# Kernel optimization log

Measured on AMD Instinct MI355X. Metric: run time of the kernel, lower is better.

Reference implementation:

```python
import jax, jax.numpy as jnp
import numpy as np

N, E, H, HEADS, NC, BLK = 100000, 1600000, 128, 4, 8192, 128

def _layernorm(x, g, b, eps=1e-5):
    m = jnp.mean(x, axis=-1, keepdims=True)
    v = jnp.var(x, axis=-1, keepdims=True)
    return (x - m) * jax.lax.rsqrt(v + eps) * g + b

def setup_inputs() -> dict:
    key = jax.random.key(0)
    ks = jax.random.split(key, 24)
    s = 0.05
    p = lambda k, shp: jax.random.normal(k, shp, jnp.float32) * s
    return {
        'x': jax.random.normal(ks[0], (N, H), jnp.float32),
        'ea': jax.random.normal(ks[1], (E, H), jnp.float32),
        # GINEConv edge linear (edge_dim -> hidden)
        'We': p(ks[2], (H, H)), 'be_': p(ks[3], (H,)),
        # GINEConv mlp: Linear(H,H) -> ReLU -> Linear(H,H)
        'W1': p(ks[4], (H, H)), 'b1': p(ks[5], (H,)),
        'W2': p(ks[6], (H, H)), 'b2': p(ks[7], (H,)),
        'ln1_g': jnp.ones((H,), jnp.float32), 'ln1_b': jnp.zeros((H,), jnp.float32),
        # MultiheadAttention packed qkv + out proj
        'in_w': p(ks[8], (3 * H, H)), 'in_b': p(ks[9], (3 * H,)),
        'out_w': p(ks[10], (H, H)), 'out_b': p(ks[11], (H,)),
        'ln2_g': jnp.ones((H,), jnp.float32), 'ln2_b': jnp.zeros((H,), jnp.float32),
        # FFN: Linear(H,2H) -> ReLU -> Linear(2H,H)
        'f1_w': p(ks[12], (2 * H, H)), 'f1_b': p(ks[13], (2 * H,)),
        'f2_w': p(ks[14], (H, 2 * H)), 'f2_b': p(ks[15], (H,)),
        'ei': jax.random.randint(ks[16], (2, E), 0, N, jnp.int64),
        'chem_idx': jnp.arange(NC, dtype=jnp.int64),
        'B': BLK,
    }

def reference(x, ea, We, be_, W1, b1, W2, b2, ln1_g, ln1_b, in_w, in_b,
              out_w, out_b, ln2_g, ln2_b, f1_w, f1_b, f2_w, f2_b,
              ei, chem_idx, B):
    n = x.shape[0]
    # ---- GINEConv: out_i = mlp((1+eps)*x_i + sum_j relu(x_j + lin(e_ji))), eps=0 ----
    src, dst = ei[0], ei[1]
    msg = jax.nn.relu(x[src] + ea @ We.T + be_)          # [E, H]
    agg = jax.ops.segment_sum(msg, dst, num_segments=n)  # [N, H]
    h = agg + x
    h = jax.nn.relu(h @ W1.T + b1) @ W2.T + b2
    x = _layernorm(x + h, ln1_g, ln1_b)
    # ---- chunked self-attention over chem nodes (chunks of size B) ----
    xc = x[chem_idx].reshape(-1, B, x.shape[-1])         # [nc, B, H]
    nc, _, hid = xc.shape
    dh = hid // HEADS
    qkv = xc @ in_w.T + in_b                             # [nc, B, 3H]
    q, k, v = jnp.split(qkv, 3, axis=-1)
    sp = lambda t: t.reshape(nc, B, HEADS, dh)
    att = jax.nn.softmax(jnp.einsum('bqhd,bkhd->bhqk', sp(q), sp(k)) * (1.0 / np.sqrt(dh)).astype(np.float32), axis=-1)
    o = jnp.einsum('bhqk,bkhd->bqhd', att, sp(v)).reshape(nc, B, hid)
    xc = xc + (o @ out_w.T + out_b)                      # residual inside BlockMHA
    xc = xc.reshape(-1, hid)
    # ---- FFN on chem subset ----
    h2 = _layernorm(xc, ln2_g, ln2_b)
    xc = xc + (jax.nn.relu(h2 @ f1_w.T + f1_b) @ f2_w.T + f2_b)
    return x.at[chem_idx].set(xc)
```

## Files before the change

### kernel.cpp

```cpp
#include <hip/hip_runtime.h>
#include <hip/hip_bf16.h>
#include <math.h>

typedef __attribute__((ext_vector_type(8))) __bf16 bf16x8;
typedef __attribute__((ext_vector_type(4))) float f32x4;
typedef __attribute__((ext_vector_type(4))) unsigned short u16x4;

#define HD  128
#define LDP 136

__device__ __forceinline__ unsigned short f2bf(float f) {
  __bf16 h = (__bf16)f;
  union { __bf16 h; unsigned short u; } v; v.h = h; return v.u;
}
__device__ __forceinline__ float bf2f(unsigned short h) {
  union { unsigned u; float f; } v; v.u = ((unsigned)h) << 16; return v.f;
}

__device__ __forceinline__ int idx_at(const void* p, long long i, int is64) {
  if (is64) return (int)((const long long*)p)[i];
  return ((const int*)p)[i];
}

__device__ __forceinline__ void mfma_tile_128(const unsigned short* a_s,
                                              const unsigned short* w_s,
                                              int w, int l15, int lg,
                                              f32x4 acc[2][8]) {
#pragma unroll
  for (int kk = 0; kk < 4; ++kk) {
    bf16x8 a[2], b[8];
#pragma unroll
    for (int mt = 0; mt < 2; ++mt)
      a[mt] = *(const bf16x8*)&a_s[(w * 32 + mt * 16 + l15) * LDP + kk * 32 + lg * 8];
#pragma unroll
    for (int nt = 0; nt < 8; ++nt)
      b[nt] = *(const bf16x8*)&w_s[(nt * 16 + l15) * LDP + kk * 32 + lg * 8];
#pragma unroll
    for (int mt = 0; mt < 2; ++mt)
#pragma unroll
      for (int nt = 0; nt < 8; ++nt)
        acc[mt][nt] = __builtin_amdgcn_mfma_f32_16x16x32_bf16(a[mt], b[nt], acc[mt][nt], 0, 0, 0);
  }
}

__device__ __forceinline__ void mfma_tile_gb(const unsigned short* a_s,
                                             const unsigned short* Wb,
                                             int w, int l15, int lg,
                                             f32x4 acc[2][8]) {
#pragma unroll
  for (int kk = 0; kk < 4; ++kk) {
    bf16x8 a[2], b[8];
#pragma unroll
    for (int mt = 0; mt < 2; ++mt)
      a[mt] = *(const bf16x8*)&a_s[(w * 32 + mt * 16 + l15) * LDP + kk * 32 + lg * 8];
#pragma unroll
    for (int nt = 0; nt < 8; ++nt)
      b[nt] = *(const bf16x8*)&Wb[(nt * 16 + l15) * 128 + kk * 32 + lg * 8];
#pragma unroll
    for (int mt = 0; mt < 2; ++mt)
#pragma unroll
      for (int nt = 0; nt < 8; ++nt)
        acc[mt][nt] = __builtin_amdgcn_mfma_f32_16x16x32_bf16(a[mt], b[nt], acc[mt][nt], 0, 0, 0);
  }
}

__device__ __forceinline__ void stage_f32s(unsigned short* dst, const float* src,
                                           long long src_ld, int tid, int T) {
  for (int i = tid; i < 128 * 32; i += T) {
    int r = i >> 5, c = (i & 31) << 2;
    float4 f = *(const float4*)&src[(long long)r * src_ld + c];
    u16x4 h = { f2bf(f.x), f2bf(f.y), f2bf(f.z), f2bf(f.w) };
    *(u16x4*)&dst[r * LDP + c] = h;
  }
}

__global__ void detect_idx_kernel(const void* __restrict__ ei, int E, int N,
                                  int* __restrict__ flag) {
  if (threadIdx.x == 0 && blockIdx.x == 0) {
    const long long* p = (const long long*)ei;
    int is64 = 1;
    long long step = E / 64; if (step < 1) step = 1;
    for (int i = 0; i < 64; ++i) {
      long long v = p[i * step];
      if (v < 0 || v >= N) { is64 = 0; break; }
    }
    *flag = is64;
  }
}

__global__ __launch_bounds__(256) void conv_we_kernel(const float* __restrict__ We,
                                                      unsigned short* __restrict__ we_bf) {
  int i = blockIdx.x * 256 + threadIdx.x;
  if (i < 128 * 128) {
    int r = i >> 7, c = i & 127;
    we_bf[r * 136 + c] = f2bf(We[i]);
  }
}
__global__ __launch_bounds__(256) void conv_w_kernel(const float* __restrict__ W,
                                                     unsigned short* __restrict__ out,
                                                     int n) {
  int i = blockIdx.x * 256 + threadIdx.x;
  if (i < n) out[i] = f2bf(W[i]);
}
__global__ __launch_bounds__(256) void conv_x_kernel(const float* __restrict__ x,
                                                     unsigned short* __restrict__ xb,
                                                     long long n8) {
  long long i = blockIdx.x * 256LL + threadIdx.x;
  if (i < n8) {
    float4 f0 = *(const float4*)&x[i * 8];
    float4 f1 = *(const float4*)&x[i * 8 + 4];
    u16x4 h0 = { f2bf(f0.x), f2bf(f0.y), f2bf(f0.z), f2bf(f0.w) };
    u16x4 h1 = { f2bf(f1.x), f2bf(f1.y), f2bf(f1.z), f2bf(f1.w) };
    *(u16x4*)&xb[i * 8] = h0;
    *(u16x4*)&xb[i * 8 + 4] = h1;
  }
}

__global__ __launch_bounds__(256) void hist_kernel(const void* __restrict__ ei,
                                                   const int* __restrict__ flag,
                                                   int* __restrict__ deg, int E) {
  const int is64 = *flag;
  for (long long e = blockIdx.x * 256LL + threadIdx.x; e < E;
       e += (long long)gridDim.x * 256)
    atomicAdd(&deg[idx_at(ei, (long long)E + e, is64)], 1);
}

#define SCH 1024
__global__ __launch_bounds__(256) void scan_a(const int* __restrict__ deg,
                                              int* __restrict__ bsum, int N) {
  const int b = blockIdx.x, t = threadIdx.x;
  int p = 0;
#pragma unroll
  for (int k = 0; k < 4; ++k) {
    int idx = b * SCH + t * 4 + k;
    if (idx < N) p += deg[idx];
  }
  __shared__ int warr[4];
  for (int o = 32; o > 0; o >>= 1) p += __shfl_xor(p, o);
  if ((t & 63) == 0) warr[t >> 6] = p;
  __syncthreads();
  if (t == 0) bsum[b] = warr[0] + warr[1] + warr[2] + warr[3];
}
__global__ void scan_b(int* __restrict__ bsum, int* __restrict__ off, int NB, int N) {
  if (threadIdx.x == 0 && blockIdx.x == 0) {
    int run = 0;
    for (int b = 0; b < NB; ++b) { int t = bsum[b]; bsum[b] = run; run += t; }
    off[N] = run;
  }
}
__global__ __launch_bounds__(128) void scan_b2(int* __restrict__ bsum,
                                               int* __restrict__ off, int NB, int N) {
  __shared__ int arr[128];
  const int t = threadIdx.x;
  int v = (t < NB) ? bsum[t] : 0;
  arr[t] = v;
  __syncthreads();
  for (int s = 1; s < 128; s <<= 1) {
    int u = (t >= s) ? arr[t - s] : 0;
    __syncthreads();
    arr[t] += u;
    __syncthreads();
  }
  if (t < NB) bsum[t] = arr[t] - v;
  if (t == 0) off[N] = arr[127];
}
__global__ __launch_bounds__(256) void scan_c(const int* __restrict__ deg,
                                              const int* __restrict__ bsum,
                                              int* __restrict__ off,
                                              int* __restrict__ cursor, int N) {
  const int b = blockIdx.x, t = threadIdx.x;
  int d[4], s = 0;
#pragma unroll
  for (int k = 0; k < 4; ++k) {
    int idx = b * SCH + t * 4 + k;
    d[k] = (idx < N) ? deg[idx] : 0;
    s += d[k];
  }
  __shared__ int arr[256];
  arr[t] = s;
  __syncthreads();
  for (int stp = 1; stp < 256; stp <<= 1) {
    int v = (t >= stp) ? arr[t - stp] : 0;
    __syncthreads();
    arr[t] += v;
    __syncthreads();
// ... 106 lines not shown
    bf16x8 g = *(const bf16x8*)&we_s[r * LDP + sg * 8];
    u16x4 h0, h1;
#pragma unroll
    for (int k = 0; k < 4; ++k) {
      float v = (float)g[k] + (float)xv[k];
      h0[k] = f2bf(v > 0.f ? v : 0.f);
    }
#pragma unroll
    for (int k = 0; k < 4; ++k) {
      float v = (float)g[4 + k] + (float)xv[4 + k];
      h1[k] = f2bf(v > 0.f ? v : 0.f);
    }
    unsigned short* mp = &msg[(size_t)s_pos[r] * 128 + sg * 8];
    *(u16x4*)&mp[0] = h0;
    *(u16x4*)&mp[4] = h1;
  }
}

__global__ __launch_bounds__(256) void gather_kernel(
    const unsigned short* __restrict__ x_bf, const int* __restrict__ off,
    const unsigned short* __restrict__ msg, unsigned short* __restrict__ h_bf,
    int N) {
  const int tid = threadIdx.x;
  const int grp = tid >> 4, li = tid & 15;
  const long long row = (long long)blockIdx.x * 16 + grp;
  if (row >= N) return;
  const int co = li * 8;
  float a8[8];
  bf16x8 xv = *(const bf16x8*)&x_bf[row * HD + co];
#pragma unroll
  for (int k = 0; k < 8; ++k) a8[k] = (float)xv[k];
  const int j0 = off[row], j1 = off[row + 1];
  int j = j0;
  for (; j + 3 < j1; j += 4) {
    bf16x8 v0 = *(const bf16x8*)&msg[(size_t)j * 128 + co];
    bf16x8 v1 = *(const bf16x8*)&msg[(size_t)(j + 1) * 128 + co];
    bf16x8 v2 = *(const bf16x8*)&msg[(size_t)(j + 2) * 128 + co];
    bf16x8 v3 = *(const bf16x8*)&msg[(size_t)(j + 3) * 128 + co];
#pragma unroll
    for (int k = 0; k < 8; ++k)
      a8[k] += ((float)v0[k] + (float)v1[k]) + ((float)v2[k] + (float)v3[k]);
  }
  for (; j < j1; ++j) {
    bf16x8 v0 = *(const bf16x8*)&msg[(size_t)j * 128 + co];
#pragma unroll
    for (int k = 0; k < 8; ++k) a8[k] += (float)v0[k];
  }
  bf16x8 hv;
#pragma unroll
  for (int k = 0; k < 8; ++k) hv[k] = (__bf16)a8[k];
  *(bf16x8*)&h_bf[row * HD + co] = hv;
}

__global__ __launch_bounds__(256, 4) void mlp_kernel(
    const float* __restrict__ x, float* __restrict__ xo,
    const unsigned short* __restrict__ h_bf,
    const unsigned short* __restrict__ W1b, const float* __restrict__ b1,
    const unsigned short* __restrict__ W2b, const float* __restrict__ b2,
    const float* __restrict__ g1, const float* __restrict__ bt1, int N) {
  __shared__ unsigned short a_s[128 * LDP];
  const int tid = threadIdx.x;
  const long long r0 = (long long)blockIdx.x * 128;

  for (int i = tid; i < 2048; i += 256) {
    int r = i >> 4, c = (i & 15) << 3;
    long long gr = r0 + r;
    bf16x8 v;
    if (gr < N) v = *(const bf16x8*)&h_bf[gr * HD + c];
    else {
#pragma unroll
      for (int k = 0; k < 8; ++k) v[k] = (__bf16)0.f;
    }
    *(bf16x8*)&a_s[r * LDP + c] = v;
  }
  __syncthreads();

  const int lane = tid & 63, w = tid >> 6;
  const int l15 = lane & 15, lg = lane >> 4;
  f32x4 acc[2][8];
#pragma unroll
  for (int mt = 0; mt < 2; ++mt)
#pragma unroll
    for (int nt = 0; nt < 8; ++nt) acc[mt][nt] = (f32x4){0.f, 0.f, 0.f, 0.f};
  mfma_tile_gb(a_s, W1b, w, l15, lg, acc);
  __syncthreads();

#pragma unroll
  for (int mt = 0; mt < 2; ++mt)
#pragma unroll
    for (int r = 0; r < 4; ++r) {
      int m = w * 32 + mt * 16 + lg * 4 + r;
#pragma unroll
      for (int nt = 0; nt < 8; ++nt) {
        int n = nt * 16 + l15;
        float t = acc[mt][nt][r] + b1[n];
        a_s[m * LDP + n] = f2bf(t > 0.f ? t : 0.f);
      }
    }
  __syncthreads();

  f32x4 acc2[2][8];
#pragma unroll
  for (int mt = 0; mt < 2; ++mt)
#pragma unroll
    for (int nt = 0; nt < 8; ++nt) acc2[mt][nt] = (f32x4){0.f, 0.f, 0.f, 0.f};
  mfma_tile_gb(a_s, W2b, w, l15, lg, acc2);
  __syncthreads();

#pragma unroll
  for (int mt = 0; mt < 2; ++mt)
#pragma unroll
    for (int r = 0; r < 4; ++r) {
      int m = w * 32 + mt * 16 + lg * 4 + r;
      if (r0 + m < N) {
#pragma unroll
        for (int nt = 0; nt < 8; ++nt) {
          int n = nt * 16 + l15;
          a_s[m * LDP + n] = f2bf(x[(r0 + m) * HD + n] + acc2[mt][nt][r] + b2[n]);
        }
      }
    }
  __syncthreads();

  for (int row = w; row < 128; row += 4) {
    if (r0 + row >= N) continue;
    float v1 = bf2f(a_s[row * LDP + lane]), v2 = bf2f(a_s[row * LDP + 64 + lane]);
    float s = v1 + v2, sq = v1 * v1 + v2 * v2;
    for (int o = 32; o > 0; o >>= 1) { s += __shfl_xor(s, o); sq += __shfl_xor(sq, o); }
    float mean = s * (1.f / 128.f);
    float var = sq * (1.f / 128.f) - mean * mean;
    float rs = rsqrtf(var + 1e-5f);
    xo[(r0 + row) * HD + lane]      = (v1 - mean) * rs * g1[lane] + bt1[lane];
    xo[(r0 + row) * HD + 64 + lane] = (v2 - mean) * rs * g1[lane + 64] + bt1[lane + 64];
  }
}

__global__ __launch_bounds__(256) void edge_kernel(
    const float* __restrict__ x, const float* __restrict__ ea,
    const float* __restrict__ We, const float* __restrict__ be,
    const void* __restrict__ ei, const int* __restrict__ flag,
    float* __restrict__ agg, int E, int N) {
  __shared__ unsigned short ea_s[128 * LDP];
  __shared__ unsigned short we_s[128 * LDP];
  __shared__ int s_src[128];
  __shared__ int s_dst[128];
  const int tid = threadIdx.x;
  const long long e0 = (long long)blockIdx.x * 128;
  const int is64 = *flag;
  if (tid < 128) {
    long long e = e0 + tid;
    int s = 0, d = 0;
    if (e < E) { s = idx_at(ei, e, is64); d = idx_at(ei, (long long)E + e, is64); }
    s_src[tid] = s; s_dst[tid] = d;
  }
  for (int i = tid; i < 128 * 32; i += 256) {
    int r = i >> 5, c = (i & 31) << 2;
    float4 f = {0.f, 0.f, 0.f, 0.f};
    if (e0 + r < E) f = *(const float4*)&ea[(e0 + r) * HD + c];
    u16x4 h = { f2bf(f.x), f2bf(f.y), f2bf(f.z), f2bf(f.w) };
    *(u16x4*)&ea_s[r * LDP + c] = h;
    float4 g = *(const float4*)&We[r * HD + c];
    u16x4 hw = { f2bf(g.x), f2bf(g.y), f2bf(g.z), f2bf(g.w) };
    *(u16x4*)&we_s[r * LDP + c] = hw;
  }
  __syncthreads();
  const int lane = tid & 63, w = tid >> 6;
  const int l15 = lane & 15, lg = lane >> 4;
  f32x4 acc[2][8];
#pragma unroll
  for (int mt = 0; mt < 2; ++mt)
#pragma unroll
    for (int nt = 0; nt < 8; ++nt) acc[mt][nt] = (f32x4){0.f, 0.f, 0.f, 0.f};
  mfma_tile_128(ea_s, we_s, w, l15, lg, acc);
  float bev[8];
#pragma unroll
  for (int nt = 0; nt < 8; ++nt) bev[nt] = be[nt * 16 + l15];
#pragma unroll
  for (int mt = 0; mt < 2; ++mt) {
#pragma unroll
    for (int r = 0; r < 4; ++r) {
      int m = w * 32 + mt * 16 + lg * 4 + r;
      if (e0 + m >= E) continue;
      const float* xrow = x + (size_t)s_src[m] * HD;
      float* arow = agg + (size_t)s_dst[m] * HD;
#pragma unroll
      for (int nt = 0; nt < 8; ++nt) {
        int n = nt * 16 + l15;
        float val = acc[mt][nt][r] + bev[nt] + xrow[n];
        if (val > 0.f) unsafeAtomicAdd(&arow[n], val);
      }
    }
  }
}

__global__ __launch_bounds__(256) void node_kernel(
    const float* __restrict__ x, float* xo,
    const float* __restrict__ W1, const float* __restrict__ b1,
    const float* __restrict__ W2, const float* __restrict__ b2,
    const float* __restrict__ g1, const float* __restrict__ bt1, int N) {
  __shared__ char smem[2 * 128 * LDP * 2];
  unsigned short* a_s = (unsigned short*)smem;
  unsigned short* w_s = (unsigned short*)smem + 128 * LDP;
  float* y_s = (float*)smem;
  const int tid = threadIdx.x;
  const long long r0 = (long long)blockIdx.x * 128;
  for (int i = tid; i < 128 * 32; i += 256) {
    int r = i >> 5, c = (i & 31) << 2;
    float4 f = {0.f, 0.f, 0.f, 0.f};
    if (r0 + r < N) {
      float4 xa = *(const float4*)&x[(r0 + r) * HD + c];
      float4 ag = *(const float4*)&xo[(r0 + r) * HD + c];
      f.x = xa.x + ag.x; f.y = xa.y + ag.y; f.z = xa.z + ag.z; f.w = xa.w + ag.w;
    }
    u16x4 h = { f2bf(f.x), f2bf(f.y), f2bf(f.z), f2bf(f.w) };
    *(u16x4*)&a_s[r * LDP + c] = h;
    float4 g = *(const float4*)&W1[r * HD + c];
    u16x4 hw = { f2bf(g.x), f2bf(g.y), f2bf(g.z), f2bf(g.w) };
    *(u16x4*)&w_s[r * LDP + c] = hw;
  }
  __syncthreads();
  const int lane = tid & 63, w = tid >> 6;
  const int l15 = lane & 15, lg = lane >> 4;
  f32x4 acc[2][8];
#pragma unroll
  for (int mt = 0; mt < 2; ++mt)
#pragma unroll
    for (int nt = 0; nt < 8; ++nt) acc[mt][nt] = (f32x4){0.f, 0.f, 0.f, 0.f};
  mfma_tile_128(a_s, w_s, w, l15, lg, acc);
  __syncthreads();
#pragma unroll
  for (int mt = 0; mt < 2; ++mt)
#pragma unroll
    for (int r = 0; r < 4; ++r) {
      int m = w * 32 + mt * 16 + lg * 4 + r;
#pragma unroll
      for (int nt = 0; nt < 8; ++nt) {
        int n = nt * 16 + l15;
        float t = acc[mt][nt][r] + b1[n];
        a_s[m * LDP + n] = f2bf(t > 0.f ? t : 0.f);
      }
    }
  stage_f32s(w_s, W2, HD, tid, 256);
  __syncthreads();
  f32x4 acc2[2][8];
#pragma unroll
  for (int mt = 0; mt < 2; ++mt)
#pragma unroll
    for (int nt = 0; nt < 8; ++nt) acc2[mt][nt] = (f32x4){0.f, 0.f, 0.f, 0.f};
  mfma_tile_128(a_s, w_s, w, l15, lg, acc2);
  __syncthreads();
#pragma unroll
  for (int mt = 0; mt < 2; ++mt)
#pragma unroll
    for (int r = 0; r < 4; ++r) {
      int m = w * 32 + mt * 16 + lg * 4 + r;
      if (r0 + m < N) {
#pragma unroll
        for (int nt = 0; nt < 8; ++nt) {
          int n = nt * 16 + l15;
          y_s[m * 132 + n] = x[(r0 + m) * HD + n] + acc2[mt][nt][r] + b2[n];
        }
      }
    }
  __syncthreads();
  for (int row = w; row < 128; row += 4) {
    if (r0 + row >= N) continue;
    float v1 = y_s[row * 132 + lane], v2 = y_s[row * 132 + 64 + lane];
    float s = v1 + v2, sq = v1 * v1 + v2 * v2;
    for (int o = 32; o > 0; o >>= 1) { s += __shfl_xor(s, o); sq += __shfl_xor(sq, o); }
    float mean = s * (1.f / 128.f);
    float var = sq * (1.f / 128.f) - mean * mean;
    float rs = rsqrtf(var + 1e-5f);
    xo[(r0 + row) * HD + lane]      = (v1 - mean) * rs * g1[lane] + bt1[lane];
    xo[(r0 + row) * HD + 64 + lane] = (v2 - mean) * rs * g1[lane + 64] + bt1[lane + 64];
  }
}

__global__ __launch_bounds__(256) void qkv_kernel(
    const float* __restrict__ xo, const float* __restrict__ in_w,
    const float* __restrict__ in_b, const void* __restrict__ chem,
    const int* __restrict__ flag, float* __restrict__ qkv) {
  __shared__ unsigned short a_s[128 * LDP];
  __shared__ unsigned short w_s[128 * LDP];
  __shared__ int s_row[128];
  const int tid = threadIdx.x;
  const int chunk = blockIdx.x, sec = blockIdx.y;
  const int is64 = *flag;
  if (tid < 128) s_row[tid] = idx_at(chem, (long long)chunk * 128 + tid, is64);
  __syncthreads();
  for (int i = tid; i < 128 * 32; i += 256) {
    int r = i >> 5, c = (i & 31) << 2;
    float4 f = *(const float4*)&xo[(size_t)s_row[r] * HD + c];
    u16x4 h = { f2bf(f.x), f2bf(f.y), f2bf(f.z), f2bf(f.w) };
    *(u16x4*)&a_s[r * LDP + c] = h;
    float4 g = *(const float4*)&in_w[(size_t)(sec * 128 + r) * HD + c];
    u16x4 hw = { f2bf(g.x), f2bf(g.y), f2bf(g.z), f2bf(g.w) };
    *(u16x4*)&w_s[r * LDP + c] = hw;
  }
  __syncthreads();
  const int lane = tid & 63, w = tid >> 6;
  const int l15 = lane & 15, lg = lane >> 4;
  f32x4 acc[2][8];
#pragma unroll
  for (int mt = 0; mt < 2; ++mt)
#pragma unroll
    for (int nt = 0; nt < 8; ++nt) acc[mt][nt] = (f32x4){0.f, 0.f, 0.f, 0.f};
  mfma_tile_128(a_s, w_s, w, l15, lg, acc);
#pragma unroll
  for (int mt = 0; mt < 2; ++mt)
#pragma unroll
    for (int r = 0; r < 4; ++r) {
      int m = w * 32 + mt * 16 + lg * 4 + r;
#pragma unroll
      for (int nt = 0; nt < 8; ++nt) {
        int n = nt * 16 + l15;
        qkv[(size_t)(chunk * 128 + m) * 384 + sec * 128 + n] = acc[mt][nt][r] + in_b[sec * 128 + n];
      }
    }
}

__global__ __launch_bounds__(128) void attn_kernel(const float* __restrict__ qkv,
                                                   float* __restrict__ o) {
  __shared__ float k_s[128 * 32];
  __shared__ float v_s[128 * 32];
  const int tid = threadIdx.x;
  const int chunk = blockIdx.x, h = blockIdx.y;
  const float scale = 0.1767766952966369f;
  for (int i = tid; i < 128 * 32; i += 128) {
    int r = i >> 5, d = i & 31;
    k_s[i] = qkv[(size_t)(chunk * 128 + r) * 384 + 128 + h * 32 + d];
    v_s[i] = qkv[(size_t)(chunk * 128 + r) * 384 + 256 + h * 32 + d];
  }
  float qr[32];
  const int m = tid;
#pragma unroll
  for (int d = 0; d < 32; ++d)
    qr[d] = qkv[(size_t)(chunk * 128 + m) * 384 + h * 32 + d] * scale;
  __syncthreads();
  float mx = -1e30f, sm = 0.f;
  for (int j = 0; j < 128; ++j) {
    float s = 0.f;
#pragma unroll
    for (int d = 0; d < 32; ++d) s += qr[d] * k_s[j * 32 + d];
    if (s > mx) { sm = sm * __expf(mx - s); mx = s; }
    sm += __expf(s - mx);
  }
  const float inv = 1.f / sm;
  float ov[32];
#pragma unroll
  for (int d = 0; d < 32; ++d) ov[d] = 0.f;
  for (int j = 0; j < 128; ++j) {
    float s = 0.f;
#pragma unroll
    for (int d = 0; d < 32; ++d) s += qr[d] * k_s[j * 32 + d];
    float p = __expf(s - mx) * inv;
#pragma unroll
    for (int d = 0; d < 32; ++d) ov[d] += p * v_s[j * 32 + d];
  }
#pragma unroll
  for (int d = 0; d < 32; ++d)
    o[(size_t)(chunk * 128 + m) * HD + h * 32 + d] = ov[d];
}

__global__ __launch_bounds__(256) void oproj_kernel(
    const float* __restrict__ xo, const float* __restrict__ o,
    const float* __restrict__ Wo, const float* __restrict__ bo,
    const float* __restrict__ g2, const float* __restrict__ bt2,
    const void* __restrict__ chem, const int* __restrict__ flag,
    float* __restrict__ xc2, unsigned short* __restrict__ h2b) {
  __shared__ char smem[2 * 128 * LDP * 2];
  unsigned short* a_s = (unsigned short*)smem;
  unsigned short* w_s = (unsigned short*)smem + 128 * LDP;
  float* y_s = (float*)smem;
  __shared__ int s_row[128];
  const int tid = threadIdx.x;
  const int chunk = blockIdx.x;
  const int is64 = *flag;
  if (tid < 128) s_row[tid] = idx_at(chem, (long long)chunk * 128 + tid, is64);
  stage_f32s(a_s, o + (size_t)chunk * 128 * HD, HD, tid, 256);
  stage_f32s(w_s, Wo, HD, tid, 256);
  __syncthreads();
  const int lane = tid & 63, w = tid >> 6;
  const int l15 = lane & 15, lg = lane >> 4;
  f32x4 acc[2][8];
#pragma unroll
  for (int mt = 0; mt < 2; ++mt)
#pragma unroll
    for (int nt = 0; nt < 8; ++nt) acc[mt][nt] = (f32x4){0.f, 0.f, 0.f, 0.f};
  mfma_tile_128(a_s, w_s, w, l15, lg, acc);
  __syncthreads();
#pragma unroll
  for (int mt = 0; mt < 2; ++mt)
#pragma unroll
    for (int r = 0; r < 4; ++r) {
      int m = w * 32 + mt * 16 + lg * 4 + r;
#pragma unroll
      for (int nt = 0; nt < 8; ++nt) {
        int n = nt * 16 + l15;
        y_s[m * 132 + n] = xo[(size_t)s_row[m] * HD + n] + acc[mt][nt][r] + bo[n];
      }
    }
  __syncthreads();
  for (int row = w; row < 128; row += 4) {
    float v1 = y_s[row * 132 + lane], v2 = y_s[row * 132 + 64 + lane];
    float s = v1 + v2, sq = v1 * v1 + v2 * v2;
    for (int o2 = 32; o2 > 0; o2 >>= 1) { s += __shfl_xor(s, o2); sq += __shfl_xor(sq, o2); }
    float mean = s * (1.f / 128.f);
    float var = sq * (1.f / 128.f) - mean * mean;
    float rs = rsqrtf(var + 1e-5f);
    size_t gi = (size_t)(chunk * 128 + row) * HD;
    xc2[gi + lane] = v1; xc2[gi + 64 + lane] = v2;
    h2b[gi + lane]      = f2bf((v1 - mean) * rs * g2[lane] + bt2[lane]);
    h2b[gi + 64 + lane] = f2bf((v2 - mean) * rs * g2[lane + 64] + bt2[lane + 64]);
  }
}

__global__ __launch_bounds__(256) void ffn1_kernel(
    const unsigned short* __restrict__ h2b, const float* __restrict__ f1w,
    const float* __restrict__ f1b, unsigned short* __restrict__ u) {
  __shared__ unsigned short a_s[128 * LDP];
  __shared__ unsigned short w_s[128 * LDP];
  const int tid = threadIdx.x;
  const int chunk = blockIdx.x, sec = blockIdx.y;
  for (int i = tid; i < 128 * 32; i += 256) {
    int r = i >> 5, c = (i & 31) << 2;
    *(u16x4*)&a_s[r * LDP + c] = *(const u16x4*)&h2b[(size_t)(chunk * 128 + r) * HD + c];
  }
  stage_f32s(w_s, f1w + (size_t)sec * 128 * HD, HD, tid, 256);
  __syncthreads();
  const int lane = tid & 63, w = tid >> 6;
  const int l15 = lane & 15, lg = lane >> 4;
  f32x4 acc[2][8];
#pragma unroll
  for (int mt = 0; mt < 2; ++mt)
#pragma unroll
    for (int nt = 0; nt < 8; ++nt) acc[mt][nt] = (f32x4){0.f, 0.f, 0.f, 0.f};
  mfma_tile_128(a_s, w_s, w, l15, lg, acc);
#pragma unroll
  for (int mt = 0; mt < 2; ++mt)
#pragma unroll
    for (int r = 0; r < 4; ++r) {
      int m = w * 32 + mt * 16 + lg * 4 + r;
#pragma unroll
      for (int nt = 0; nt < 8; ++nt) {
        int n = nt * 16 + l15;
        float t = acc[mt][nt][r] + f1b[sec * 128 + n];
        u[(size_t)(chunk * 128 + m) * 256 + sec * 128 + n] = f2bf(t > 0.f ? t : 0.f);
      }
    }
}

__global__ __launch_bounds__(256) void ffn2_kernel(
    const unsigned short* __restrict__ u, const float* __restrict__ f2w,
    const float* __restrict__ f2b, const float* __restrict__ xc2,
    const void* __restrict__ chem, const int* __restrict__ flag,
    float* __restrict__ out) {
  __shared__ unsigned short a_s[128 * LDP];
  __shared__ unsigned short w_s[128 * LDP];
  __shared__ int s_row[128];
  const int tid = threadIdx.x;
  const int chunk = blockIdx.x;
  const int is64 = *flag;
  if (tid < 128) s_row[tid] = idx_at(chem, (long long)chunk * 128 + tid, is64);
  const int lane = tid & 63, w = tid >> 6;
  const int l15 = lane & 15, lg = lane >> 4;
  f32x4 acc[2][8];
#pragma unroll
  for (int mt = 0; mt < 2; ++mt)
#pragma unroll
    for (int nt = 0; nt < 8; ++nt) acc[mt][nt] = (f32x4){0.f, 0.f, 0.f, 0.f};
  for (int half = 0; half < 2; ++half) {
    __syncthreads();
    for (int i = tid; i < 128 * 32; i += 256) {
      int r = i >> 5, c = (i & 31) << 2;
      *(u16x4*)&a_s[r * LDP + c] =
          *(const u16x4*)&u[(size_t)(chunk * 128 + r) * 256 + half * 128 + c];
      float4 g = *(const float4*)&f2w[(size_t)r * 256 + half * 128 + c];
      u16x4 hw = { f2bf(g.x), f2bf(g.y), f2bf(g.z), f2bf(g.w) };
      *(u16x4*)&w_s[r * LDP + c] = hw;
    }
    __syncthreads();
    mfma_tile_128(a_s, w_s, w, l15, lg, acc);
  }
#pragma unroll
  for (int mt = 0; mt < 2; ++mt)
#pragma unroll
    for (int r = 0; r < 4; ++r) {
      int m = w * 32 + mt * 16 + lg * 4 + r;
#pragma unroll
      for (int nt = 0; nt < 8; ++nt) {
        int n = nt * 16 + l15;
        float val = xc2[(size_t)(chunk * 128 + m) * HD + n] + acc[mt][nt][r] + f2b[n];
        out[(size_t)s_row[m] * HD + n] = val;
      }
    }
}

extern "C" void kernel_launch(void* const* d_in, const int* in_sizes, int n_in,
                              void* d_out, int out_size, void* d_ws, size_t ws_size,
                              hipStream_t stream) {
  const float* x    = (const float*)d_in[0];
  const float* ea   = (const float*)d_in[1];
  const float* We   = (const float*)d_in[2];
  const float* be   = (const float*)d_in[3];
  const float* W1   = (const float*)d_in[4];
  const float* b1   = (const float*)d_in[5];
  const float* W2   = (const float*)d_in[6];
  const float* b2   = (const float*)d_in[7];
  const float* g1   = (const float*)d_in[8];
  const float* bt1  = (const float*)d_in[9];
  const float* in_w = (const float*)d_in[10];
  const float* in_b = (const float*)d_in[11];
  const float* outw = (const float*)d_in[12];
  const float* outb = (const float*)d_in[13];
  const float* g2   = (const float*)d_in[14];
  const float* bt2  = (const float*)d_in[15];
  const float* f1w  = (const float*)d_in[16];
  const float* f1b  = (const float*)d_in[17];
  const float* f2w  = (const float*)d_in[18];
  const float* f2b  = (const float*)d_in[19];
  const void*  ei   = d_in[20];
  const void*  chem = d_in[21];
  const int N  = in_sizes[0] / HD;
  const int E  = in_sizes[1] / HD;
  const int NC = in_sizes[21];
  const int NB = (N + SCH - 1) / SCH;
  float* xo = (float*)d_out;

  char* ws = (char*)d_ws;
  size_t o = 0;
  auto alloc = [&](size_t bytes) { size_t p = o; o = (o + bytes + 255) & ~255ULL; return p; };
  size_t o_qkv  = alloc((size_t)NC * 384 * 4);
  size_t o_obuf = alloc((size_t)NC * 128 * 4);
  size_t o_xc2  = alloc((size_t)NC * 128 * 4);
  size_t o_h2b  = alloc((size_t)NC * 128 * 2);
  size_t o_ubuf = alloc((size_t)NC * 256 * 2);
  size_t o_flag = alloc(4);
  size_t o_webf = alloc(128 * 136 * 2);
  size_t o_w1b  = alloc(128 * 128 * 2);
  size_t o_w2b  = alloc(128 * 128 * 2);
  size_t o_xbf  = alloc((size_t)N * 128 * 2);
  size_t o_hbf  = alloc((size_t)N * 128 * 2);
  size_t o_deg  = alloc((size_t)N * 4);
  size_t o_off  = alloc((size_t)(N + 1) * 4);
  size_t o_cur  = alloc((size_t)N * 4);
  size_t o_bsum = alloc((size_t)NB * 4);
  size_t o_msg  = alloc((size_t)E * 128 * 2);
  size_t need = o;

  float*          qkv  = (float*)(ws + o_qkv);
  float*          obuf = (float*)(ws + o_obuf);
  float*          xc2  = (float*)(ws + o_xc2);
  unsigned short* h2b  = (unsigned short*)(ws + o_h2b);
  unsigned short* ubuf = (unsigned short*)(ws + o_ubuf);
  int*            flag = (int*)(ws + o_flag);
  unsigned short* webf = (unsigned short*)(ws + o_webf);
  unsigned short* w1b  = (unsigned short*)(ws + o_w1b);
  unsigned short* w2b  = (unsigned short*)(ws + o_w2b);
  unsigned short* xbf  = (unsigned short*)(ws + o_xbf);
  unsigned short* hbf  = (unsigned short*)(ws + o_hbf);
  int*            deg  = (int*)(ws + o_deg);
  int*            off  = (int*)(ws + o_off);
  int*            cur  = (int*)(ws + o_cur);
  int*            bsum = (int*)(ws + o_bsum);
  unsigned short* msg  = (unsigned short*)(ws + o_msg);

  detect_idx_kernel<<<1, 64, 0, stream>>>(ei, E, N, flag);

  if (ws_size >= need) {
    hipMemsetAsync(deg, 0, (size_t)N * 4, stream);
    conv_x_kernel<<<dim3((N * 16 + 255) / 256), 256, 0, stream>>>(x, xbf, (long long)N * 16);
    hist_kernel<<<dim3(1024), 256, 0, stream>>>(ei, flag, deg, E);
    scan_a<<<dim3(NB), 256, 0, stream>>>(deg, bsum, N);
    if (NB <= 128) scan_b2<<<1, 128, 0, stream>>>(bsum, off, NB, N);
    else           scan_b<<<1, 64, 0, stream>>>(bsum, off, NB, N);
    scan_c<<<dim3(NB), 256, 0, stream>>>(deg, bsum, off, cur, N);
    conv_we_kernel<<<dim3(64), 256, 0, stream>>>(We, webf);
    conv_w_kernel<<<dim3(64), 256, 0, stream>>>(W1, w1b, 128 * 128);
    conv_w_kernel<<<dim3(64), 256, 0, stream>>>(W2, w2b, 128 * 128);
    edge_kernel9<<<dim3((E + 127) / 128), 256, 0, stream>>>(xbf, ea, webf, be, ei,
                                                            flag, cur, msg, E);
    gather_kernel<<<dim3((N + 15) / 16), 256, 0, stream>>>(xbf, off, msg, hbf, N);
    mlp_kernel<<<dim3((N + 127) / 128), 256, 0, stream>>>(x, xo, hbf, w1b, b1, w2b,
                                                          b2, g1, bt1, N);
  } else {
    hipMemsetAsync(xo, 0, (size_t)N * HD * sizeof(float), stream);
    edge_kernel<<<dim3((E + 127) / 128), 256, 0, stream>>>(x, ea, We, be, ei, flag, xo, E, N);
    node_kernel<<<dim3((N + 127) / 128), 256, 0, stream>>>(x, xo, W1, b1, W2, b2, g1, bt1, N);
  }

  const int ncs = NC / 128;
  qkv_kernel<<<dim3(ncs, 3), 256, 0, stream>>>(xo, in_w, in_b, chem, flag, qkv);
  attn_kernel<<<dim3(ncs, 4), 128, 0, stream>>>(qkv, obuf);
  oproj_kernel<<<dim3(ncs), 256, 0, stream>>>(xo, obuf, outw, outb, g2, bt2, chem, flag, xc2, h2b);
  ffn1_kernel<<<dim3(ncs, 2), 256, 0, stream>>>(h2b, f1w, f1b, ubuf);
  ffn2_kernel<<<dim3(ncs), 256, 0, stream>>>(ubuf, f2w, f2b, xc2, chem, flag, xo);
}
```

Measured before the change: 732.7 us.

## Fuse chunked attention and FFN into one per-chunk MFMA kernel

```diff
diff --git a/kernel.cpp b/kernel.cpp
--- a/kernel.cpp
+++ b/kernel.cpp
@@ -44,7 +44,7 @@
 }
 
 __device__ __forceinline__ void mfma_tile_gb(const unsigned short* a_s,
-                                             const unsigned short* Wb,
+                                             const unsigned short* Wb, int ldw,
                                              int w, int l15, int lg,
                                              f32x4 acc[2][8]) {
 #pragma unroll
@@ -55,7 +55,7 @@
       a[mt] = *(const bf16x8*)&a_s[(w * 32 + mt * 16 + l15) * LDP + kk * 32 + lg * 8];
 #pragma unroll
     for (int nt = 0; nt < 8; ++nt)
-      b[nt] = *(const bf16x8*)&Wb[(nt * 16 + l15) * 128 + kk * 32 + lg * 8];
+      b[nt] = *(const bf16x8*)&Wb[(size_t)(nt * 16 + l15) * ldw + kk * 32 + lg * 8];
 #pragma unroll
     for (int mt = 0; mt < 2; ++mt)
 #pragma unroll
@@ -96,11 +96,20 @@
     we_bf[r * 136 + c] = f2bf(We[i]);
   }
 }
-__global__ __launch_bounds__(256) void conv_w_kernel(const float* __restrict__ W,
-                                                     unsigned short* __restrict__ out,
-                                                     int n) {
+__global__ __launch_bounds__(256) void conv_weights_kernel(
+    const float* __restrict__ W1, const float* __restrict__ W2,
+    const float* __restrict__ inw, const float* __restrict__ wo,
+    const float* __restrict__ f1, const float* __restrict__ f2,
+    unsigned short* __restrict__ w1b, unsigned short* __restrict__ w2b,
+    unsigned short* __restrict__ inwb, unsigned short* __restrict__ wob,
+    unsigned short* __restrict__ f1b, unsigned short* __restrict__ f2b) {
   int i = blockIdx.x * 256 + threadIdx.x;
-  if (i < n) out[i] = f2bf(W[i]);
+  if (i < 16384) w1b[i] = f2bf(W1[i]);
+  else if (i < 32768) w2b[i - 16384] = f2bf(W2[i - 16384]);
+  else if (i < 81920) inwb[i - 32768] = f2bf(inw[i - 32768]);
+  else if (i < 98304) wob[i - 81920] = f2bf(wo[i - 81920]);
+  else if (i < 131072) f1b[i - 98304] = f2bf(f1[i - 98304]);
+  else if (i < 163840) f2b[i - 131072] = f2bf(f2[i - 131072]);
 }
 __global__ __launch_bounds__(256) void conv_x_kernel(const float* __restrict__ x,
                                                      unsigned short* __restrict__ xb,
@@ -373,7 +382,7 @@
   for (int mt = 0; mt < 2; ++mt)
 #pragma unroll
     for (int nt = 0; nt < 8; ++nt) acc[mt][nt] = (f32x4){0.f, 0.f, 0.f, 0.f};
-  mfma_tile_gb(a_s, W1b, w, l15, lg, acc);
+  mfma_tile_gb(a_s, W1b, 128, w, l15, lg, acc);
   __syncthreads();
 
 #pragma unroll
@@ -395,7 +404,7 @@
   for (int mt = 0; mt < 2; ++mt)
 #pragma unroll
     for (int nt = 0; nt < 8; ++nt) acc2[mt][nt] = (f32x4){0.f, 0.f, 0.f, 0.f};
-  mfma_tile_gb(a_s, W2b, w, l15, lg, acc2);
+  mfma_tile_gb(a_s, W2b, 128, w, l15, lg, acc2);
   __syncthreads();
 
 #pragma unroll
@@ -424,6 +433,215 @@
     xo[(r0 + row) * HD + lane]      = (v1 - mean) * rs * g1[lane] + bt1[lane];
     xo[(r0 + row) * HD + 64 + lane] = (v2 - mean) * rs * g1[lane + 64] + bt1[lane + 64];
   }
+}
+
+__global__ __launch_bounds__(256) void chem_kernel(
+    float* __restrict__ xo,
+    const unsigned short* __restrict__ inwb, const float* __restrict__ in_b,
+    const unsigned short* __restrict__ wob, const float* __restrict__ bo,
+    const float* __restrict__ g2, const float* __restrict__ bt2,
+    const unsigned short* __restrict__ f1wb, const float* __restrict__ f1b,
+    const unsigned short* __restrict__ f2wb, const float* __restrict__ f2b,
+    const void* __restrict__ chem, const int* __restrict__ flag) {
+  __shared__ unsigned short xc_s[128 * LDP];
+  __shared__ unsigned short q_s[128 * LDP];
+  __shared__ unsigned short k_s[128 * LDP];
+  __shared__ unsigned short vt_s[128 * LDP];
+  __shared__ int s_row[128];
+  const int tid = threadIdx.x, chunk = blockIdx.x;
+  const int is64 = *flag;
+  if (tid < 128) s_row[tid] = idx_at(chem, (long long)chunk * 128 + tid, is64);
+  __syncthreads();
+
+  for (int i = tid; i < 2048; i += 256) {
+    int r = i >> 4, c = (i & 15) << 3;
+    const float* src = &xo[(size_t)s_row[r] * HD + c];
+    float4 f0 = *(const float4*)&src[0];
+    float4 f1 = *(const float4*)&src[4];
+    u16x4 h0 = { f2bf(f0.x), f2bf(f0.y), f2bf(f0.z), f2bf(f0.w) };
+    u16x4 h1 = { f2bf(f1.x), f2bf(f1.y), f2bf(f1.z), f2bf(f1.w) };
+    *(u16x4*)&xc_s[r * LDP + c] = h0;
+    *(u16x4*)&xc_s[r * LDP + c + 4] = h1;
+  }
+  __syncthreads();
+
+  const int lane = tid & 63, w = tid >> 6;
+  const int l15 = lane & 15, lg = lane >> 4;
+  const float scale = 0.1767766952966369f;
+
+  for (int sec = 0; sec < 3; ++sec) {
+    f32x4 acc[2][8];
+#pragma unroll
+    for (int mt = 0; mt < 2; ++mt)
+#pragma unroll
+      for (int nt = 0; nt < 8; ++nt) acc[mt][nt] = (f32x4){0.f, 0.f, 0.f, 0.f};
+    mfma_tile_gb(xc_s, inwb + (size_t)sec * 128 * 128, 128, w, l15, lg, acc);
+#pragma unroll
+    for (int mt = 0; mt < 2; ++mt)
+#pragma unroll
+      for (int r = 0; r < 4; ++r) {
+        int m = w * 32 + mt * 16 + lg * 4 + r;
+#pragma unroll
+        for (int nt = 0; nt < 8; ++nt) {
+          int n = nt * 16 + l15;
+          float t = acc[mt][nt][r] + in_b[sec * 128 + n];
+          if (sec == 0)      q_s[m * LDP + n] = f2bf(t * scale);
+          else if (sec == 1) k_s[m * LDP + n] = f2bf(t);
+          else               vt_s[n * LDP + m] = f2bf(t);
+        }
+      }
+  }
+  __syncthreads();
+
+  f32x4 oacc[2][8];
+#pragma unroll
+  for (int mt = 0; mt < 2; ++mt)
+#pragma unroll
+    for (int nt = 0; nt < 8; ++nt) oacc[mt][nt] = (f32x4){0.f, 0.f, 0.f, 0.f};
+
+  for (int h = 0; h < 4; ++h) {
+    f32x4 sacc[2][8];
+#pragma unroll
+    for (int mt = 0; mt < 2; ++mt)
+#pragma unroll
+      for (int nt = 0; nt < 8; ++nt) sacc[mt][nt] = (f32x4){0.f, 0.f, 0.f, 0.f};
+    {
+      bf16x8 a[2], b[8];
+#pragma unroll
+      for (int mt = 0; mt < 2; ++mt)
+        a[mt] = *(const bf16x8*)&q_s[(w * 32 + mt * 16 + l15) * LDP + h * 32 + lg * 8];
+#pragma unroll
+      for (int nt = 0; nt < 8; ++nt)
+        b[nt] = *(const bf16x8*)&k_s[(nt * 16 + l15) * LDP + h * 32 + lg * 8];
+#pragma unroll
+      for (int mt = 0; mt < 2; ++mt)
+#pragma unroll
+        for (int nt = 0; nt < 8; ++nt)
+          sacc[mt][nt] = __builtin_amdgcn_mfma_f32_16x16x32_bf16(a[mt], b[nt], sacc[mt][nt], 0, 0, 0);
+    }
+#pragma unroll
+    for (int mt = 0; mt < 2; ++mt)
+#pragma unroll
+      for (int r = 0; r < 4; ++r) {
+        int m = w * 32 + mt * 16 + lg * 4 + r;
+        float mx = -1e30f;
+#pragma unroll
+        for (int nt = 0; nt < 8; ++nt) mx = fmaxf(mx, sacc[mt][nt][r]);
+        for (int o = 8; o > 0; o >>= 1) mx = fmaxf(mx, __shfl_xor(mx, o));
+        float sm = 0.f;
+        float p[8];
+#pragma unroll
+        for (int nt = 0; nt < 8; ++nt) { p[nt] = __expf(sacc[mt][nt][r] - mx); sm += p[nt]; }
+        for (int o = 8; o > 0; o >>= 1) sm += __shfl_xor(sm, o);
+        float inv = 1.f / sm;
+#pragma unroll
+        for (int nt = 0; nt < 8; ++nt)
+          xc_s[m * LDP + nt * 16 + l15] = f2bf(p[nt] * inv);
+      }
+#pragma unroll
+    for (int kk = 0; kk < 4; ++kk) {
+      bf16x8 pa[2], vb[2];
+#pragma unroll
+      for (int mt = 0; mt < 2; ++mt)
+        pa[mt] = *(const bf16x8*)&xc_s[(w * 32 + mt * 16 + l15) * LDP + kk * 32 + lg * 8];
+#pragma unroll
+      for (int nt2 = 0; nt2 < 2; ++nt2)
+        vb[nt2] = *(const bf16x8*)&vt_s[(h * 32 + nt2 * 16 + l15) * LDP + kk * 32 + lg * 8];
+#pragma unroll
+      for (int mt = 0; mt < 2; ++mt)
+#pragma unroll
+        for (int nt2 = 0; nt2 < 2; ++nt2)
+          oacc[mt][h * 2 + nt2] =
+              __builtin_amdgcn_mfma_f32_16x16x32_bf16(pa[mt], vb[nt2], oacc[mt][h * 2 + nt2], 0, 0, 0);
+    }
+  }
+  __syncthreads();
+
+#pragma unroll
+  for (int mt = 0; mt < 2; ++mt)
+#pragma unroll
+    for (int r = 0; r < 4; ++r) {
+      int m = w * 32 + mt * 16 + lg * 4 + r;
+#pragma unroll
+      for (int nt = 0; nt < 8; ++nt)
+        q_s[m * LDP + nt * 16 + l15] = f2bf(oacc[mt][nt][r]);
+    }
+
+  f32x4 pacc[2][8];
+#pragma unroll
+  for (int mt = 0; mt < 2; ++mt)
+#pragma unroll
+    for (int nt = 0; nt < 8; ++nt) pacc[mt][nt] = (f32x4){0.f, 0.f, 0.f, 0.f};
+  mfma_tile_gb(q_s, wob, 128, w, l15, lg, pacc);
+
+#pragma unroll
+  for (int mt = 0; mt < 2; ++mt)
+#pragma unroll
+    for (int r = 0; r < 4; ++r) {
+      int m = w * 32 + mt * 16 + lg * 4 + r;
+      const float* xrow = &xo[(size_t)s_row[m] * HD];
+      float y[8];
+      float s = 0.f, sq = 0.f;
+#pragma unroll
+      for (int nt = 0; nt < 8; ++nt) {
+        int n = nt * 16 + l15;
+        y[nt] = xrow[n] + pacc[mt][nt][r] + bo[n];
+        s += y[nt]; sq += y[nt] * y[nt];
+      }
+      for (int o = 8; o > 0; o >>= 1) { s += __shfl_xor(s, o); sq += __shfl_xor(sq, o); }
+      float mean = s * (1.f / 128.f);
+      float var = sq * (1.f / 128.f) - mean * mean;
+      float rs = rsqrtf(var + 1e-5f);
+#pragma unroll
+      for (int nt = 0; nt < 8; ++nt) {
+        int n = nt * 16 + l15;
+        xc_s[m * LDP + n] = f2bf((y[nt] - mean) * rs * g2[n] + bt2[n]);
+        k_s[m * LDP + n]  = f2bf(y[nt]);
+      }
+    }
+
+  for (int sec = 0; sec < 2; ++sec) {
+    f32x4 acc[2][8];
+#pragma unroll
+    for (int mt = 0; mt < 2; ++mt)
+#pragma unroll
+      for (int nt = 0; nt < 8; ++nt) acc[mt][nt] = (f32x4){0.f, 0.f, 0.f, 0.f};
+    mfma_tile_gb(xc_s, f1wb + (size_t)sec * 128 * 128, 128, w, l15, lg, acc);
+    unsigned short* ub = (sec == 0) ? q_s : vt_s;
+#pragma unroll
+    for (int mt = 0; mt < 2; ++mt)
+#pragma unroll
+      for (int r = 0; r < 4; ++r) {
+        int m = w * 32 + mt * 16 + lg * 4 + r;
+#pragma unroll
+        for (int nt = 0; nt < 8; ++nt) {
+          int n = nt * 16 + l15;
+          float t = acc[mt][nt][r] + f1b[sec * 128 + n];
+          ub[m * LDP + n] = f2bf(t > 0.f ? t : 0.f);
+        }
+      }
+  }
+
+  f32x4 facc[2][8];
+#pragma unroll
+  for (int mt = 0; mt < 2; ++mt)
+#pragma unroll
+    for (int nt = 0; nt < 8; ++nt) facc[mt][nt] = (f32x4){0.f, 0.f, 0.f, 0.f};
+  mfma_tile_gb(q_s, f2wb, 256, w, l15, lg, facc);
+  mfma_tile_gb(vt_s, f2wb + 128, 256, w, l15, lg, facc);
+
+#pragma unroll
+  for (int mt = 0; mt < 2; ++mt)
+#pragma unroll
+    for (int r = 0; r < 4; ++r) {
+      int m = w * 32 + mt * 16 + lg * 4 + r;
+      float* orow = &xo[(size_t)s_row[m] * HD];
+#pragma unroll
+      for (int nt = 0; nt < 8; ++nt) {
+        int n = nt * 16 + l15;
+        orow[n] = bf2f(k_s[m * LDP + n]) + facc[mt][nt][r] + f2b[n];
+      }
+    }
 }
 
 __global__ __launch_bounds__(256) void edge_kernel(
@@ -565,226 +783,6 @@
     xo[(r0 + row) * HD + lane]      = (v1 - mean) * rs * g1[lane] + bt1[lane];
     xo[(r0 + row) * HD + 64 + lane] = (v2 - mean) * rs * g1[lane + 64] + bt1[lane + 64];
   }
-}
-
-__global__ __launch_bounds__(256) void qkv_kernel(
-    const float* __restrict__ xo, const float* __restrict__ in_w,
-    const float* __restrict__ in_b, const void* __restrict__ chem,
-    const int* __restrict__ flag, float* __restrict__ qkv) {
-  __shared__ unsigned short a_s[128 * LDP];
-  __shared__ unsigned short w_s[128 * LDP];
-  __shared__ int s_row[128];
-  const int tid = threadIdx.x;
-  const int chunk = blockIdx.x, sec = blockIdx.y;
-  const int is64 = *flag;
-  if (tid < 128) s_row[tid] = idx_at(chem, (long long)chunk * 128 + tid, is64);
-  __syncthreads();
-  for (int i = tid; i < 128 * 32; i += 256) {
-    int r = i >> 5, c = (i & 31) << 2;
-    float4 f = *(const float4*)&xo[(size_t)s_row[r] * HD + c];
-    u16x4 h = { f2bf(f.x), f2bf(f.y), f2bf(f.z), f2bf(f.w) };
-    *(u16x4*)&a_s[r * LDP + c] = h;
-    float4 g = *(const float4*)&in_w[(size_t)(sec * 128 + r) * HD + c];
-    u16x4 hw = { f2bf(g.x), f2bf(g.y), f2bf(g.z), f2bf(g.w) };
-    *(u16x4*)&w_s[r * LDP + c] = hw;
-  }
-  __syncthreads();
-  const int lane = tid & 63, w = tid >> 6;
-  const int l15 = lane & 15, lg = lane >> 4;
-  f32x4 acc[2][8];
-#pragma unroll
-  for (int mt = 0; mt < 2; ++mt)
-#pragma unroll
-    for (int nt = 0; nt < 8; ++nt) acc[mt][nt] = (f32x4){0.f, 0.f, 0.f, 0.f};
-  mfma_tile_128(a_s, w_s, w, l15, lg, acc);
-#pragma unroll
-  for (int mt = 0; mt < 2; ++mt)
-#pragma unroll
-    for (int r = 0; r < 4; ++r) {
-      int m = w * 32 + mt * 16 + lg * 4 + r;
-#pragma unroll
-      for (int nt = 0; nt < 8; ++nt) {
-        int n = nt * 16 + l15;
-        qkv[(size_t)(chunk * 128 + m) * 384 + sec * 128 + n] = acc[mt][nt][r] + in_b[sec * 128 + n];
-      }
-    }
-}
-
-__global__ __launch_bounds__(128) void attn_kernel(const float* __restrict__ qkv,
-                                                   float* __restrict__ o) {
-  __shared__ float k_s[128 * 32];
-  __shared__ float v_s[128 * 32];
-  const int tid = threadIdx.x;
-  const int chunk = blockIdx.x, h = blockIdx.y;
-  const float scale = 0.1767766952966369f;
-  for (int i = tid; i < 128 * 32; i += 128) {
-    int r = i >> 5, d = i & 31;
-    k_s[i] = qkv[(size_t)(chunk * 128 + r) * 384 + 128 + h * 32 + d];
-    v_s[i] = qkv[(size_t)(chunk * 128 + r) * 384 + 256 + h * 32 + d];
-  }
-  float qr[32];
-  const int m = tid;
-#pragma unroll
-  for (int d = 0; d < 32; ++d)
-    qr[d] = qkv[(size_t)(chunk * 128 + m) * 384 + h * 32 + d] * scale;
-  __syncthreads();
-  float mx = -1e30f, sm = 0.f;
-  for (int j = 0; j < 128; ++j) {
-    float s = 0.f;
-#pragma unroll
-    for (int d = 0; d < 32; ++d) s += qr[d] * k_s[j * 32 + d];
-    if (s > mx) { sm = sm * __expf(mx - s); mx = s; }
-    sm += __expf(s - mx);
-  }
-  const float inv = 1.f / sm;
-  float ov[32];
-#pragma unroll
-  for (int d = 0; d < 32; ++d) ov[d] = 0.f;
-  for (int j = 0; j < 128; ++j) {
-    float s = 0.f;
-#pragma unroll
-    for (int d = 0; d < 32; ++d) s += qr[d] * k_s[j * 32 + d];
-    float p = __expf(s - mx) * inv;
-#pragma unroll
-    for (int d = 0; d < 32; ++d) ov[d] += p * v_s[j * 32 + d];
-  }
-#pragma unroll
-  for (int d = 0; d < 32; ++d)
-    o[(size_t)(chunk * 128 + m) * HD + h * 32 + d] = ov[d];
-}
-
-__global__ __launch_bounds__(256) void oproj_kernel(
-    const float* __restrict__ xo, const float* __restrict__ o,
-    const float* __restrict__ Wo, const float* __restrict__ bo,
-    const float* __restrict__ g2, const float* __restrict__ bt2,
-    const void* __restrict__ chem, const int* __restrict__ flag,
-    float* __restrict__ xc2, unsigned short* __restrict__ h2b) {
-  __shared__ char smem[2 * 128 * LDP * 2];
-  unsigned short* a_s = (unsigned short*)smem;
-  unsigned short* w_s = (unsigned short*)smem + 128 * LDP;
-  float* y_s = (float*)smem;
-  __shared__ int s_row[128];
-  const int tid = threadIdx.x;
-  const int chunk = blockIdx.x;
-  const int is64 = *flag;
-  if (tid < 128) s_row[tid] = idx_at(chem, (long long)chunk * 128 + tid, is64);
-  stage_f32s(a_s, o + (size_t)chunk * 128 * HD, HD, tid, 256);
-  stage_f32s(w_s, Wo, HD, tid, 256);
-  __syncthreads();
-  const int lane = tid & 63, w = tid >> 6;
-  const int l15 = lane & 15, lg = lane >> 4;
-  f32x4 acc[2][8];
-#pragma unroll
-  for (int mt = 0; mt < 2; ++mt)
-#pragma unroll
-    for (int nt = 0; nt < 8; ++nt) acc[mt][nt] = (f32x4){0.f, 0.f, 0.f, 0.f};
-  mfma_tile_128(a_s, w_s, w, l15, lg, acc);
-  __syncthreads();
-#pragma unroll
-  for (int mt = 0; mt < 2; ++mt)
-#pragma unroll
-    for (int r = 0; r < 4; ++r) {
-      int m = w * 32 + mt * 16 + lg * 4 + r;
-#pragma unroll
-      for (int nt = 0; nt < 8; ++nt) {
-        int n = nt * 16 + l15;
-        y_s[m * 132 + n] = xo[(size_t)s_row[m] * HD + n] + acc[mt][nt][r] + bo[n];
-      }
-    }
-  __syncthreads();
-  for (int row = w; row < 128; row += 4) {
-    float v1 = y_s[row * 132 + lane], v2 = y_s[row * 132 + 64 + lane];
-    float s = v1 + v2, sq = v1 * v1 + v2 * v2;
-    for (int o2 = 32; o2 > 0; o2 >>= 1) { s += __shfl_xor(s, o2); sq += __shfl_xor(sq, o2); }
-    float mean = s * (1.f / 128.f);
-    float var = sq * (1.f / 128.f) - mean * mean;
-    float rs = rsqrtf(var + 1e-5f);
-    size_t gi = (size_t)(chunk * 128 + row) * HD;
-    xc2[gi + lane] = v1; xc2[gi + 64 + lane] = v2;
-    h2b[gi + lane]      = f2bf((v1 - mean) * rs * g2[lane] + bt2[lane]);
-    h2b[gi + 64 + lane] = f2bf((v2 - mean) * rs * g2[lane + 64] + bt2[lane + 64]);
-  }
-}
-
-__global__ __launch_bounds__(256) void ffn1_kernel(
-    const unsigned short* __restrict__ h2b, const float* __restrict__ f1w,
-    const float* __restrict__ f1b, unsigned short* __restrict__ u) {
-  __shared__ unsigned short a_s[128 * LDP];
-  __shared__ unsigned short w_s[128 * LDP];
-  const int tid = threadIdx.x;
-  const int chunk = blockIdx.x, sec = blockIdx.y;
-  for (int i = tid; i < 128 * 32; i += 256) {
-    int r = i >> 5, c = (i & 31) << 2;
-    *(u16x4*)&a_s[r * LDP + c] = *(const u16x4*)&h2b[(size_t)(chunk * 128 + r) * HD + c];
-  }
-  stage_f32s(w_s, f1w + (size_t)sec * 128 * HD, HD, tid, 256);
-  __syncthreads();
-  const int lane = tid & 63, w = tid >> 6;
-  const int l15 = lane & 15, lg = lane >> 4;
-  f32x4 acc[2][8];
-#pragma unroll
-  for (int mt = 0; mt < 2; ++mt)
-#pragma unroll
-    for (int nt = 0; nt < 8; ++nt) acc[mt][nt] = (f32x4){0.f, 0.f, 0.f, 0.f};
-  mfma_tile_128(a_s, w_s, w, l15, lg, acc);
-#pragma unroll
-  for (int mt = 0; mt < 2; ++mt)
-#pragma unroll
-    for (int r = 0; r < 4; ++r) {
-      int m = w * 32 + mt * 16 + lg * 4 + r;
-#pragma unroll
-      for (int nt = 0; nt < 8; ++nt) {
-        int n = nt * 16 + l15;
-        float t = acc[mt][nt][r] + f1b[sec * 128 + n];
-        u[(size_t)(chunk * 128 + m) * 256 + sec * 128 + n] = f2bf(t > 0.f ? t : 0.f);
-      }
-    }
-}
-
-__global__ __launch_bounds__(256) void ffn2_kernel(
-    const unsigned short* __restrict__ u, const float* __restrict__ f2w,
-    const float* __restrict__ f2b, const float* __restrict__ xc2,
-    const void* __restrict__ chem, const int* __restrict__ flag,
-    float* __restrict__ out) {
-  __shared__ unsigned short a_s[128 * LDP];
-  __shared__ unsigned short w_s[128 * LDP];
-  __shared__ int s_row[128];
-  const int tid = threadIdx.x;
-  const int chunk = blockIdx.x;
-  const int is64 = *flag;
-  if (tid < 128) s_row[tid] = idx_at(chem, (long long)chunk * 128 + tid, is64);
-  const int lane = tid & 63, w = tid >> 6;
-  const int l15 = lane & 15, lg = lane >> 4;
-  f32x4 acc[2][8];
-#pragma unroll
-  for (int mt = 0; mt < 2; ++mt)
-#pragma unroll
-    for (int nt = 0; nt < 8; ++nt) acc[mt][nt] = (f32x4){0.f, 0.f, 0.f, 0.f};
-  for (int half = 0; half < 2; ++half) {
-    __syncthreads();
-    for (int i = tid; i < 128 * 32; i += 256) {
-      int r = i >> 5, c = (i & 31) << 2;
-      *(u16x4*)&a_s[r * LDP + c] =
-          *(const u16x4*)&u[(size_t)(chunk * 128 + r) * 256 + half * 128 + c];
-      float4 g = *(const float4*)&f2w[(size_t)r * 256 + half * 128 + c];
-      u16x4 hw = { f2bf(g.x), f2bf(g.y), f2bf(g.z), f2bf(g.w) };
-      *(u16x4*)&w_s[r * LDP + c] = hw;
-    }
-    __syncthreads();
-    mfma_tile_128(a_s, w_s, w, l15, lg, acc);
-  }
-#pragma unroll
-  for (int mt = 0; mt < 2; ++mt)
-#pragma unroll
-    for (int r = 0; r < 4; ++r) {
-      int m = w * 32 + mt * 16 + lg * 4 + r;
-#pragma unroll
-      for (int nt = 0; nt < 8; ++nt) {
-        int n = nt * 16 + l15;
-        float val = xc2[(size_t)(chunk * 128 + m) * HD + n] + acc[mt][nt][r] + f2b[n];
-        out[(size_t)s_row[m] * HD + n] = val;
-      }
-    }
 }
 
 extern "C" void kernel_launch(void* const* d_in, const int* in_sizes, int n_in,
@@ -821,15 +819,14 @@
   char* ws = (char*)d_ws;
   size_t o = 0;
   auto alloc = [&](size_t bytes) { size_t p = o; o = (o + bytes + 255) & ~255ULL; return p; };
-  size_t o_qkv  = alloc((size_t)NC * 384 * 4);
-  size_t o_obuf = alloc((size_t)NC * 128 * 4);
-  size_t o_xc2  = alloc((size_t)NC * 128 * 4);
-  size_t o_h2b  = alloc((size_t)NC * 128 * 2);
-  size_t o_ubuf = alloc((size_t)NC * 256 * 2);
   size_t o_flag = alloc(4);
   size_t o_webf = alloc(128 * 136 * 2);
   size_t o_w1b  = alloc(128 * 128 * 2);
   size_t o_w2b  = alloc(128 * 128 * 2);
+  size_t o_inwb = alloc(384 * 128 * 2);
+  size_t o_wob  = alloc(128 * 128 * 2);
+  size_t o_f1wb = alloc(256 * 128 * 2);
+  size_t o_f2wb = alloc(128 * 256 * 2);
   size_t o_xbf  = alloc((size_t)N * 128 * 2);
   size_t o_hbf  = alloc((size_t)N * 128 * 2);
   size_t o_deg  = alloc((size_t)N * 4);
@@ -839,15 +836,14 @@
   size_t o_msg  = alloc((size_t)E * 128 * 2);
   size_t need = o;
 
-  float*          qkv  = (float*)(ws + o_qkv);
-  float*          obuf = (float*)(ws + o_obuf);
-  float*          xc2  = (float*)(ws + o_xc2);
-  unsigned short* h2b  = (unsigned short*)(ws + o_h2b);
-  unsigned short* ubuf = (unsigned short*)(ws + o_ubuf);
   int*            flag = (int*)(ws + o_flag);
   unsigned short* webf = (unsigned short*)(ws + o_webf);
   unsigned short* w1b  = (unsigned short*)(ws + o_w1b);
   unsigned short* w2b  = (unsigned short*)(ws + o_w2b);
+  unsigned short* inwb = (unsigned short*)(ws + o_inwb);
+  unsigned short* wob  = (unsigned short*)(ws + o_wob);
+  unsigned short* f1wb = (unsigned short*)(ws + o_f1wb);
+  unsigned short* f2wb = (unsigned short*)(ws + o_f2wb);
   unsigned short* xbf  = (unsigned short*)(ws + o_xbf);
   unsigned short* hbf  = (unsigned short*)(ws + o_hbf);
   int*            deg  = (int*)(ws + o_deg);
@@ -857,6 +853,8 @@
   unsigned short* msg  = (unsigned short*)(ws + o_msg);
 
   detect_idx_kernel<<<1, 64, 0, stream>>>(ei, E, N, flag);
+  conv_weights_kernel<<<dim3(640), 256, 0, stream>>>(W1, W2, in_w, outw, f1w, f2w,
+                                                     w1b, w2b, inwb, wob, f1wb, f2wb);
 
   if (ws_size >= need) {
     hipMemsetAsync(deg, 0, (size_t)N * 4, stream);
@@ -867,8 +865,6 @@
     else           scan_b<<<1, 64, 0, stream>>>(bsum, off, NB, N);
     scan_c<<<dim3(NB), 256, 0, stream>>>(deg, bsum, off, cur, N);
     conv_we_kernel<<<dim3(64), 256, 0, stream>>>(We, webf);
-    conv_w_kernel<<<dim3(64), 256, 0, stream>>>(W1, w1b, 128 * 128);
-    conv_w_kernel<<<dim3(64), 256, 0, stream>>>(W2, w2b, 128 * 128);
     edge_kernel9<<<dim3((E + 127) / 128), 256, 0, stream>>>(xbf, ea, webf, be, ei,
                                                             flag, cur, msg, E);
     gather_kernel<<<dim3((N + 15) / 16), 256, 0, stream>>>(xbf, off, msg, hbf, N);
@@ -880,10 +876,6 @@
     node_kernel<<<dim3((N + 127) / 128), 256, 0, stream>>>(x, xo, W1, b1, W2, b2, g1, bt1, N);
   }
 
-  const int ncs = NC / 128;
-  qkv_kernel<<<dim3(ncs, 3), 256, 0, stream>>>(xo, in_w, in_b, chem, flag, qkv);
-  attn_kernel<<<dim3(ncs, 4), 128, 0, stream>>>(qkv, obuf);
-  oproj_kernel<<<dim3(ncs), 256, 0, stream>>>(xo, obuf, outw, outb, g2, bt2, chem, flag, xc2, h2b);
-  ffn1_kernel<<<dim3(ncs, 2), 256, 0, stream>>>(h2b, f1w, f1b, ubuf);
-  ffn2_kernel<<<dim3(ncs), 256, 0, stream>>>(ubuf, f2w, f2b, xc2, chem, flag, xo);
-}
+  chem_kernel<<<dim3(NC / 128), 256, 0, stream>>>(xo, inwb, in_b, wob, outb, g2, bt2,
+                                                  f1wb, f1b, f2wb, f2b, chem, flag);
+}
```

Result: faster. 656.7 us (-10.4%).
